# Performance work log

Measured on AMD Instinct MI355X. Metric: run time of the kernel, lower is better.

The kernel has to match this reference:

```python
import jax, jax.numpy as jnp
import numpy as np

LN_EPS = 1e-5

def layer_norm(x, g, b):
    m = x.mean(-1, keepdims=True)
    v = ((x - m) ** 2).mean(-1, keepdims=True)
    return (x - m) / jnp.sqrt(v + LN_EPS) * g + b

def gat_conv(x, src, dst, W, att_src, att_dst, bias, heads, out_ch, concat):
    # PyG GATConv (eval mode, self-loops already included in src/dst).
    N = x.shape[0]
    h = (x @ W).reshape(N, heads, out_ch)                 # [N,H,C]
    a_src = (h * att_src).sum(-1)                          # [N,H]
    a_dst = (h * att_dst).sum(-1)                          # [N,H]
    e = jax.nn.leaky_relu(a_src[src] + a_dst[dst], 0.2)   # [E,H]
    emax = jax.ops.segment_max(e, dst, num_segments=N)    # [N,H]
    ee = jnp.exp(e - emax[dst])
    denom = jax.ops.segment_sum(ee, dst, num_segments=N)  # [N,H]
    alpha = ee / (denom[dst] + 1e-16)                      # [E,H]
    out = jax.ops.segment_sum(alpha[:, :, None] * h[src], dst, num_segments=N)  # [N,H,C]
    out = out.reshape(N, heads * out_ch) if concat else out.mean(axis=1)
    return out + bias

def setup_inputs() -> dict:
    key = jax.random.key(0)
    ks = jax.random.split(key, 32)
    N, G, E = 50000, 405, 300000
    RH, GH, H = 256, 256, 4
    def w(k, shape, fan_in):
        return jax.random.normal(k, shape, dtype=jnp.float32) * (1.0 / np.sqrt(fan_in))
    d = {}
    d["x"] = jax.random.normal(ks[0], (N, G), dtype=jnp.float32)
    d["edge_index"] = jax.random.randint(ks[1], (2, E), 0, N, dtype=jnp.int64)
    # JointEncoder
    d["enc_w1"] = w(ks[2], (G, RH), G); d["enc_b1"] = jnp.zeros(RH)
    d["ln1_g"] = jnp.ones(RH); d["ln1_b"] = jnp.zeros(RH)
    d["enc_w2"] = w(ks[3], (RH, RH), RH); d["enc_b2"] = jnp.zeros(RH)
    d["ln2_g"] = jnp.ones(RH); d["ln2_b"] = jnp.zeros(RH)
    d["w1"] = w(ks[4], (RH, H * GH), RH)
    d["att_src1"] = w(ks[5], (H, GH), GH); d["att_dst1"] = w(ks[6], (H, GH), GH)
    d["bias1"] = jnp.zeros(H * GH)
    d["res1_w"] = w(ks[7], (RH, H * GH), RH); d["res1_b"] = jnp.zeros(H * GH)
    d["w2"] = w(ks[8], (H * GH, 2 * 96), H * GH)
    d["att_src2"] = w(ks[9], (2, 96), 96); d["att_dst2"] = w(ks[10], (2, 96), 96)
    d["bias2"] = jnp.zeros(2 * 96)
    d["res2_w"] = w(ks[11], (H * GH, 2 * 96), H * GH); d["res2_b"] = jnp.zeros(2 * 96)
    d["w3"] = w(ks[12], (192, 128), 192)
    d["att_src3"] = w(ks[13], (1, 128), 128); d["att_dst3"] = w(ks[14], (1, 128), 128)
    d["bias3"] = jnp.zeros(128)
    d["res3_w"] = w(ks[15], (192, 128), 192); d["res3_b"] = jnp.zeros(128)
    # MLP head
    d["mlp_w1"] = w(ks[16], (128, 64), 128); d["mlp_b1"] = jnp.zeros(64)
    d["mlp_w2"] = w(ks[17], (64, 2), 64); d["mlp_b2"] = jnp.zeros(2)
    return d

def reference(x, edge_index, enc_w1, enc_b1, ln1_g, ln1_b, enc_w2, enc_b2, ln2_g, ln2_b,
              w1, att_src1, att_dst1, bias1, res1_w, res1_b,
              w2, att_src2, att_dst2, bias2, res2_w, res2_b,
              w3, att_src3, att_dst3, bias3, res3_w, res3_b,
              mlp_w1, mlp_b1, mlp_w2, mlp_b2):
    N = x.shape[0]
    loop = jnp.arange(N, dtype=edge_index.dtype)
    src = jnp.concatenate([edge_index[0], loop])
    dst = jnp.concatenate([edge_index[1], loop])
    # JointEncoder (eval: dropout is identity)
    h = jax.nn.relu(layer_norm(x @ enc_w1 + enc_b1, ln1_g, ln1_b))
    h = jax.nn.relu(layer_norm(h @ enc_w2 + enc_b2, ln2_g, ln2_b))
    # Block 1
    idn = h
    h = jax.nn.elu(gat_conv(h, src, dst, w1, att_src1, att_dst1, bias1, 4, 256, True))
    h = h + (idn @ res1_w + res1_b)
    # Block 2
    idn = h
    h = jax.nn.elu(gat_conv(h, src, dst, w2, att_src2, att_dst2, bias2, 2, 96, True))
    h = h + (idn @ res2_w + res2_b)
    # Block 3
    idn = h
    h = jax.nn.elu(gat_conv(h, src, dst, w3, att_src3, att_dst3, bias3, 1, 128, False))
    h = h + (idn @ res3_w + res3_b)
    # MLP head
    out = jax.nn.relu(h @ mlp_w1 + mlp_b1) @ mlp_w2 + mlp_b2
    return out
```

## Files before the change

kernel.cpp:

```cpp
#include <hip/hip_runtime.h>
#include <cstddef>

#define LN_EPS 1e-5f

typedef __bf16 bf16x8 __attribute__((ext_vector_type(8)));
typedef float  f32x4  __attribute__((ext_vector_type(4)));

typedef __attribute__((address_space(3))) unsigned int lds_u32;
typedef __attribute__((address_space(1))) unsigned int glb_u32;

__device__ __forceinline__ void gl2lds16(const void* g, void* l) {
    __builtin_amdgcn_global_load_lds((const glb_u32*)g, (lds_u32*)l, 16, 0, 0);
}

__device__ __forceinline__ float b2f(ushort h) {
    return __uint_as_float(((unsigned)h) << 16);
}
__device__ __forceinline__ ushort f2b(float f) {
    unsigned u = __float_as_uint(f);
    return (ushort)((u + 0x7fffu + ((u >> 16) & 1u)) >> 16);
}
__device__ __forceinline__ unsigned pack2(float lo, float hi) {
    return (unsigned)f2b(lo) | ((unsigned)f2b(hi) << 16);
}
__device__ __forceinline__ uint2 pack4(const f32x4 v) {
    return make_uint2(pack2(v[0], v[1]), pack2(v[2], v[3]));
}

__device__ __forceinline__ void xcd_map(int& bx, int& by) {
    int NX = gridDim.x, MBr = gridDim.y;
    int L = blockIdx.y * NX + blockIdx.x;
    int G = NX * 8;
    int g = L / G;
    if (g * 8 + 8 <= MBr) {
        int r = L - g * G;
        by = g * 8 + (r & 7);
        bx = r >> 3;
    } else {
        by = L / NX;
        bx = L - by * NX;
    }
}

__device__ __forceinline__ float wave_allreduce_max(float v) {
    #pragma unroll
    for (int off = 32; off > 0; off >>= 1) v = fmaxf(v, __shfl_xor(v, off, 64));
    return v;
}
__device__ __forceinline__ float wave_allreduce_sum(float v) {
    #pragma unroll
    for (int off = 32; off > 0; off >>= 1) v += __shfl_xor(v, off, 64);
    return v;
}

__device__ __forceinline__ void stage3(const ushort* a0, const ushort* a1, const ushort* b0,
                                       ushort* __restrict__ As, ushort* __restrict__ Bs,
                                       int lb) {
    gl2lds16(a0, As + lb);
    gl2lds16(a1, As + lb + 4096);
    gl2lds16(b0, Bs + lb);
}

__device__ __forceinline__ void mfma_loop256(const ushort* aA0, const ushort* aA1,
                                             const ushort* aB0,
                                             ushort* __restrict__ As, ushort* __restrict__ Bs,
                                             int lb,
                                             int K, int wr, int wc, int cA, int l15,
                                             f32x4 acc[4][4]) {
    const int BUFA = 256 * 32;
    const int BUFB = 128 * 32;
    const int nk = K >> 5;
    stage3(aA0, aA1, aB0, As, Bs, lb);
    int p = 0;
    for (int t = 0; t < nk; t++) {
        asm volatile("s_waitcnt vmcnt(0)" ::: "memory");
        __builtin_amdgcn_s_barrier();
        __builtin_amdgcn_sched_barrier(0);
        int kn = (t + 1) * 32;
        if (kn < K) stage3(aA0 + kn, aA1 + kn, aB0 + kn,
                           As + (p ^ 1) * BUFA, Bs + (p ^ 1) * BUFB, lb);
        const ushort* Ac = As + p * BUFA;
        const ushort* Bc = Bs + p * BUFB;
        bf16x8 af[4], bf[4];
        #pragma unroll
        for (int i = 0; i < 4; i++)
            af[i] = *reinterpret_cast<const bf16x8*>(&Ac[(wr + i * 16 + l15) * 32 + cA]);
        #pragma unroll
        for (int j = 0; j < 4; j++)
            bf[j] = *reinterpret_cast<const bf16x8*>(&Bc[(wc + j * 16 + l15) * 32 + cA]);
        #pragma unroll
        for (int i = 0; i < 4; i++)
            #pragma unroll
            for (int j = 0; j < 4; j++)
                acc[i][j] = __builtin_amdgcn_mfma_f32_16x16x32_bf16(bf[j], af[i], acc[i][j], 0, 0, 0);
        p ^= 1;
    }
    __syncthreads();
}

template<int EPI>
__global__ __launch_bounds__(512, 4) void bgemm(const ushort* __restrict__ A,
                                                const ushort* __restrict__ BT,
                                                const float* __restrict__ bias,
                                                void* __restrict__ out, int ldc,
                                                float* __restrict__ Rf,
                                                float* __restrict__ Sf, int Fs,
                                                int M, int Ncols, int K, int lda) {
    __shared__ ushort As[2][256 * 32];
    __shared__ ushort Bs[2][128 * 32];
    const int tid = threadIdx.x;
    int bx, by; xcd_map(bx, by);
    const int m0 = by * 256, n0 = bx * 128;
    const int w = tid >> 6, lane = tid & 63;
    const int wr = (w >> 1) * 64, wc = (w & 1) * 64;
    const int quad = lane >> 4, l15 = lane & 15;
    const int cA = (quad ^ ((l15 >> 1) & 3)) * 8;
    const int lb = w * 512;

    const int r = tid >> 2, g = ((tid & 3) ^ ((tid >> 3) & 3)) * 8;
    int ga0 = m0 + r;       if (ga0 >= M) ga0 = M - 1;
    int ga1 = m0 + 128 + r; if (ga1 >= M) ga1 = M - 1;
    const ushort* aA0 = A + (size_t)ga0 * lda + g;
    const ushort* aA1 = A + (size_t)ga1 * lda + g;
    const ushort* aB0 = BT + (size_t)(n0 + r) * K + g;

    f32x4 acc[4][4] = {};
    mfma_loop256(aA0, aA1, aB0, As[0], Bs[0], lb, K, wr, wc, cA, l15, acc);

    if (EPI == 4) {
        if (wc == 0) {
            #pragma unroll
            for (int i = 0; i < 4; i++) {
                float o0 = 0.f, o1 = 0.f;
                #pragma unroll
                for (int j = 0; j < 4; j++) {
                    int colbase = j * 16 + quad * 4;
                    float4 bv = *reinterpret_cast<const float4*>(&bias[colbase]);
                    float bb[4] = { bv.x, bv.y, bv.z, bv.w };
                    #pragma unroll
                    for (int rr = 0; rr < 4; rr++) {
                        float vv = fmaxf(acc[i][j][rr] + bb[rr], 0.f);
                        int c = colbase + rr;
                        o0 += vv * Rf[2 * c];
                        o1 += vv * Rf[2 * c + 1];
                    }
                }
                o0 += __shfl_xor(o0, 16, 64); o0 += __shfl_xor(o0, 32, 64);
                o1 += __shfl_xor(o1, 16, 64); o1 += __shfl_xor(o1, 32, 64);
                int row = m0 + wr + i * 16 + l15;
                if (quad == 0 && row < M) {
                    ((float*)out)[(size_t)row * 2]     = o0 + Sf[0];
                    ((float*)out)[(size_t)row * 2 + 1] = o1 + Sf[1];
                }
            }
        }
        return;
    }

    const int twoH = Ncols - 2 * Fs;
    #pragma unroll
    for (int i = 0; i < 4; i++) {
        int row = m0 + wr + i * 16 + l15;
        if (row >= M) continue;
        #pragma unroll
        for (int j = 0; j < 4; j++) {
            int colbase = n0 + wc + j * 16 + quad * 4;
            if (EPI == 0) {
                f32x4 v = acc[i][j];
                if (bias) {
                    float4 bv = *reinterpret_cast<const float4*>(&bias[colbase]);
                    v[0] += bv.x; v[1] += bv.y; v[2] += bv.z; v[3] += bv.w;
                }
                *reinterpret_cast<f32x4*>(&((float*)out)[(size_t)row * ldc + colbase]) = v;
            } else if (EPI == 5) {
                if (colbase + 3 < Fs) {
                    *reinterpret_cast<uint2*>(&((ushort*)out)[(size_t)row * Fs + colbase]) = pack4(acc[i][j]);
                } else if (colbase >= Fs && colbase + 3 < 2 * Fs) {
                    *reinterpret_cast<f32x4*>(&Rf[(size_t)row * Fs + (colbase - Fs)]) = acc[i][j];
                } else {
                    #pragma unroll
                    for (int rr = 0; rr < 4; rr++) {
                        int col = colbase + rr;
                        if (col < 2 * Fs || col >= Ncols) continue;
                        Sf[(size_t)row * twoH + (col - 2 * Fs)] = acc[i][j][rr];
                    }
                }
            }
        }
    }
}

__global__ __launch_bounds__(512, 4) void bgemm_b1(const ushort* __restrict__ accb,
                                                   const ushort* __restrict__ w1T,
                                                   const ushort* __restrict__ h1b,
                                                   const ushort* __restrict__ res1T,
                                                   const float* __restrict__ bias1,
                                                   const float* __restrict__ res1b,
                                                   ushort* __restrict__ H2b, int M) {
    __shared__ ushort As[2][256 * 32];
    __shared__ ushort Bs[2][128 * 32];
    const int tid = threadIdx.x;
    int bx, by; xcd_map(bx, by);
    const int m0 = by * 256, n0 = bx * 128;
    const int h = n0 >> 8;
    const int w = tid >> 6, lane = tid & 63;
    const int wr = (w >> 1) * 64, wc = (w & 1) * 64;
    const int quad = lane >> 4, l15 = lane & 15;
    const int cA = (quad ^ ((l15 >> 1) & 3)) * 8;
    const int lb = w * 512;

    const int r = tid >> 2, g = ((tid & 3) ^ ((tid >> 3) & 3)) * 8;
    int ga0 = m0 + r;       if (ga0 >= M) ga0 = M - 1;
    int ga1 = m0 + 128 + r; if (ga1 >= M) ga1 = M - 1;

    f32x4 acc[4][4] = {};

    mfma_loop256(accb + (size_t)ga0 * 1024 + h * 256 + g,
                 accb + (size_t)ga1 * 1024 + h * 256 + g,
                 w1T + (size_t)(n0 + r) * 256 + g,
                 As[0], Bs[0], lb, 256, wr, wc, cA, l15, acc);

    #pragma unroll
    for (int i = 0; i < 4; i++) {
        #pragma unroll
        for (int j = 0; j < 4; j++) {
            int colbase = n0 + wc + j * 16 + quad * 4;
            float4 bv = *reinterpret_cast<const float4*>(&bias1[colbase]);
            float4 rv = *reinterpret_cast<const float4*>(&res1b[colbase]);
            float bb[4] = { bv.x, bv.y, bv.z, bv.w };
            float rr[4] = { rv.x, rv.y, rv.z, rv.w };
            #pragma unroll
            for (int q = 0; q < 4; q++) {
                float t = acc[i][j][q] + bb[q];
                t = t > 0.f ? t : (__expf(t) - 1.f);
                acc[i][j][q] = t + rr[q];
            }
        }
    }

    mfma_loop256(h1b + (size_t)ga0 * 256 + g,
                 h1b + (size_t)ga1 * 256 + g,
                 res1T + (size_t)(n0 + r) * 256 + g,
                 As[0], Bs[0], lb, 256, wr, wc, cA, l15, acc);

    #pragma unroll
    for (int i = 0; i < 4; i++) {
        int row = m0 + wr + i * 16 + l15;
        if (row >= M) continue;
        #pragma unroll
        for (int j = 0; j < 4; j++) {
            int colbase = n0 + wc + j * 16 + quad * 4;
            *reinterpret_cast<uint2*>(&H2b[(size_t)row * 1024 + colbase]) = pack4(acc[i][j]);
        }
    }
}

__global__ void conv_pad_x_kernel(const float* __restrict__ x, ushort* __restrict__ xb, int N) {
    int t = blockIdx.x * 256 + threadIdx.x;
    if (t >= N * 448) return;
    int n = t / 448, k = t - n * 448;
    xb[t] = f2b(k < 405 ? x[(size_t)n * 405 + k] : 0.f);
}

#define PREP_PB 5135
__device__ __forceinline__ void prep_seg(int t, const float* src, ushort* dst,
                                         int K, int Nreal, int Kpad, int ldsrc) {
    int n = t / Kpad, k = t - n * Kpad;
    float v = (k < K && n < Nreal) ? src[(size_t)k * ldsrc + n] : 0.f;
    dst[t] = f2b(v);
}

__global__ void prep_fold_kernel(const float* __restrict__ enc_w1, const float* __restrict__ enc_w2,
                                 const float* __restrict__ w1, const float* __restrict__ res1_w,
                                 const float* __restrict__ w2, const float* __restrict__ res2_w,
                                 const float* __restrict__ w3, const float* __restrict__ res3_w,
                                 const float* __restrict__ mlp_w1,
                                 const float* __restrict__ att_s1, const float* __restrict__ att_d1,
                                 const float* __restrict__ att_s2, const float* __restrict__ att_d2,
                                 const float* __restrict__ att_s3, const float* __restrict__ att_d3,
                                 ushort* __restrict__ enc_w1T, ushort* __restrict__ enc_w2T,
                                 ushort* __restrict__ w1T, ushort* __restrict__ res1T,
                                 ushort* __restrict__ Bcat2T, ushort* __restrict__ Bcat3T,
                                 ushort* __restrict__ mlpw1T,
                                 float* __restrict__ qs, float* __restrict__ qd) {
    int blk = blockIdx.x;
    if (blk < PREP_PB) {
        int t = blk * 256 + threadIdx.x;
        const int c0 = 114688;
        const int c1 = c0 + 65536;
        const int c2 = c1 + 262144;
        const int c3 = c2 + 262144;
        const int c4 = c3 + 196608;
        const int c5 = c4 + 196608;
        const int c6 = c5 + 126976;
        const int c7 = c6 + 24576;
        const int c8 = c7 + 24576;
        const int c9 = c8 + 24192;
        const int c10 = c9 + 16384;
        if (t < c0)      prep_seg(t,        enc_w1, enc_w1T, 405, 256, 448, 256);
        else if (t < c1) prep_seg(t - c0,   enc_w2, enc_w2T, 256, 256, 256, 256);
        else if (t < c2) prep_seg(t - c1,   w1,     w1T,     256, 1024, 256, 1024);
        else if (t < c3) prep_seg(t - c2,   res1_w, res1T,   256, 1024, 256, 1024);
        else if (t < c4) prep_seg(t - c3,   w2,     Bcat2T,  1024, 192, 1024, 192);
        else if (t < c5) prep_seg(t - c4,   res2_w, Bcat2T + (size_t)192 * 1024, 1024, 192, 1024, 192);
        else if (t < c6) Bcat2T[(size_t)388 * 1024 + (t - c5)] = 0;
        else if (t < c7) prep_seg(t - c6,   w3,     Bcat3T,  192, 128, 192, 128);
        else if (t < c8) prep_seg(t - c7,   res3_w, Bcat3T + (size_t)128 * 192, 192, 128, 192, 128);
        else if (t < c9) Bcat3T[(size_t)258 * 192 + (t - c8)] = 0;
        else if (t < c10) prep_seg(t - c9,  mlp_w1, mlpw1T,  128, 64, 128, 64);
        return;
    }
    int fw = (blk - PREP_PB) * 4 + (threadIdx.x >> 6);
    int lane = threadIdx.x & 63;
    if (fw < 1024) {
        int h = fw >> 8, k = fw & 255;
        const float* wrow = w1 + (size_t)k * 1024 + h * 256;
        f32x4 wv = *reinterpret_cast<const f32x4*>(&wrow[lane * 4]);
        f32x4 as = *reinterpret_cast<const f32x4*>(&att_s1[h * 256 + lane * 4]);
        f32x4 ad = *reinterpret_cast<const f32x4*>(&att_d1[h * 256 + lane * 4]);
        float ss = wv[0] * as[0] + wv[1] * as[1] + wv[2] * as[2] + wv[3] * as[3];
        float sd = wv[0] * ad[0] + wv[1] * ad[1] + wv[2] * ad[2] + wv[3] * ad[3];
        ss = wave_allreduce_sum(ss);
        sd = wave_allreduce_sum(sd);
        if (lane == 0) { qs[fw] = ss; qd[fw] = sd; }
    } else if (fw < 1024 + 2048) {
        int t = fw - 1024;
        int h = t >> 10, k = t & 1023;
        const float* wrow = w2 + (size_t)k * 192 + h * 96;
        const float* as = att_s2 + h * 96;
        const float* ad = att_d2 + h * 96;
        float w0 = wrow[lane];
        float ss = w0 * as[lane], sd = w0 * ad[lane];
        if (lane < 32) {
            float w1v = wrow[64 + lane];
            ss += w1v * as[64 + lane];
            sd += w1v * ad[64 + lane];
        }
        ss = wave_allreduce_sum(ss);
        sd = wave_allreduce_sum(sd);
        if (lane == 0) {
            Bcat2T[(size_t)384 * 1024 + t] = f2b(ss);
            Bcat2T[(size_t)386 * 1024 + t] = f2b(sd);
        }
    } else {
        int t = fw - 3072;
        if (t < 192) {
            const float* wrow = w3 + (size_t)t * 128;
            float w0 = wrow[lane], w1v = wrow[64 + lane];
            float ss = w0 * att_s3[lane] + w1v * att_s3[64 + lane];
            float sd = w0 * att_d3[lane] + w1v * att_d3[64 + lane];
            ss = wave_allreduce_sum(ss);
            sd = wave_allreduce_sum(sd);
            if (lane == 0) {
                Bcat3T[(size_t)256 * 192 + t] = f2b(ss);
                Bcat3T[(size_t)257 * 192 + t] = f2b(sd);
            }
        }
    }
}

template<int H>
__global__ __launch_bounds__(256) void ln_relu_w_kernel(const float* __restrict__ x,
                                                        const float* __restrict__ g,
                                                        const float* __restrict__ b,
                                                        const float* __restrict__ qs,
                                                        const float* __restrict__ qd,
                                                        ushort* __restrict__ out,
                                                        float* __restrict__ a_s,
                                                        float* __restrict__ a_d,
                                                        int N) {
    const int lane = threadIdx.x & 63;
    int wid = blockIdx.x * 4 + (threadIdx.x >> 6);
    const int nw = gridDim.x * 4;
    const int c4 = lane * 4;

    f32x4 gv = *reinterpret_cast<const f32x4*>(&g[c4]);
    f32x4 bv = *reinterpret_cast<const f32x4*>(&b[c4]);
    f32x4 qsv[H > 0 ? H : 1], qdv[H > 0 ? H : 1];
    if (H > 0) {
        #pragma unroll
        for (int hh = 0; hh < H; hh++) {
            qsv[hh] = *reinterpret_cast<const f32x4*>(&qs[hh * 256 + c4]);
            qdv[hh] = *reinterpret_cast<const f32x4*>(&qd[hh * 256 + c4]);
        }
    }

    for (int r0 = wid * 2; r0 < N; r0 += 2 * nw) {
        int r1 = r0 + 1;
        bool has1 = r1 < N;
        f32x4 va = *reinterpret_cast<const f32x4*>(&x[(size_t)r0 * 256 + c4]);
        f32x4 vb = has1 ? *reinterpret_cast<const f32x4*>(&x[(size_t)r1 * 256 + c4]) : va;
        float sa  = va[0] + va[1] + va[2] + va[3];
        float s2a = va[0] * va[0] + va[1] * va[1] + va[2] * va[2] + va[3] * va[3];
        float sb  = vb[0] + vb[1] + vb[2] + vb[3];
        float s2b = vb[0] * vb[0] + vb[1] * vb[1] + vb[2] * vb[2] + vb[3] * vb[3];
        #pragma unroll
        for (int off = 32; off > 0; off >>= 1) {
            sa  += __shfl_xor(sa,  off, 64);
            sb  += __shfl_xor(sb,  off, 64);
            s2a += __shfl_xor(s2a, off, 64);
            s2b += __shfl_xor(s2b, off, 64);
        }
        float ma  = sa * (1.f / 256.f);
        float mb  = sb * (1.f / 256.f);
        float rsa = rsqrtf(s2a * (1.f / 256.f) - ma * ma + LN_EPS);
        float rsb = rsqrtf(s2b * (1.f / 256.f) - mb * mb + LN_EPS);
        f32x4 oa, ob;
        #pragma unroll
        for (int k = 0; k < 4; k++) {
            oa[k] = fmaxf((va[k] - ma) * rsa * gv[k] + bv[k], 0.f);
            ob[k] = fmaxf((vb[k] - mb) * rsb * gv[k] + bv[k], 0.f);
        }
        *reinterpret_cast<uint2*>(&out[(size_t)r0 * 256 + c4]) =
            make_uint2(pack2(oa[0], oa[1]), pack2(oa[2], oa[3]));
        if (has1)
            *reinterpret_cast<uint2*>(&out[(size_t)r1 * 256 + c4]) =
                make_uint2(pack2(ob[0], ob[1]), pack2(ob[2], ob[3]));
        if (H > 0) {
            float sc[H > 0 ? 4 * H : 1];
            #pragma unroll
            for (int hh = 0; hh < H; hh++) {
                sc[hh]           = oa[0] * qsv[hh][0] + oa[1] * qsv[hh][1] + oa[2] * qsv[hh][2] + oa[3] * qsv[hh][3];
                sc[H + hh]       = oa[0] * qdv[hh][0] + oa[1] * qdv[hh][1] + oa[2] * qdv[hh][2] + oa[3] * qdv[hh][3];
                sc[2 * H + hh]   = ob[0] * qsv[hh][0] + ob[1] * qsv[hh][1] + ob[2] * qsv[hh][2] + ob[3] * qsv[hh][3];
                sc[3 * H + hh]   = ob[0] * qdv[hh][0] + ob[1] * qdv[hh][1] + ob[2] * qdv[hh][2] + ob[3] * qdv[hh][3];
            }
            #pragma unroll
            for (int off = 32; off > 0; off >>= 1)
                #pragma unroll
                for (int k = 0; k < 4 * H; k++) sc[k] += __shfl_xor(sc[k], off, 64);
            if (lane == 0) {
                #pragma unroll
                for (int k = 0; k < H; k++) a_s[(size_t)r0 * H + k] = sc[k];
                if (has1)
                    #pragma unroll
                    for (int k = 0; k < H; k++) a_s[(size_t)r1 * H + k] = sc[2 * H + k];
            } else if (lane == 1) {
                #pragma unroll
                for (int k = 0; k < H; k++) a_d[(size_t)r0 * H + k] = sc[H + k];
                if (has1)
                    #pragma unroll
                    for (int k = 0; k < H; k++) a_d[(size_t)r1 * H + k] = sc[3 * H + k];
            }
        }
    }
}

__device__ __forceinline__ void edge_sd(const int* ei, int e, int E, int& s, int& d) {
    if (e < E) { s = ei[e]; d = ei[E + e]; } else { s = d = e - E; }
}

__global__ void deg_kernel(const int* __restrict__ ei, int* __restrict__ deg, int E, int Et) {
    int e = blockIdx.x * blockDim.x + threadIdx.x;
    if (e >= Et) return;
    int s, d; edge_sd(ei, e, E, s, d);
    atomicAdd(&deg[d], 1);
}

__global__ __launch_bounds__(256) void scan1_kernel(const int* __restrict__ deg,
                                                    int* __restrict__ incl,
                                                    int* __restrict__ part, int N) {
    __shared__ int sd[256];
    int t = threadIdx.x;
    int i = blockIdx.x * 256 + t;
    int v = (i < N) ? deg[i] : 0;
    sd[t] = v; __syncthreads();
    #pragma unroll
    for (int o = 1; o < 256; o <<= 1) {
        int x = (t >= o) ? sd[t - o] : 0;
        __syncthreads();
        sd[t] += x;
        __syncthreads();
    }
    if (i < N) incl[i] = sd[t];
    if (t == 255) part[blockIdx.x] = sd[255];
}

__global__ __launch_bounds__(256) void scan2_kernel(int* __restrict__ part, int nb) {
    __shared__ int sd[256];
    int t = threadIdx.x;
    int v = (t < nb) ? part[t] : 0;
    sd[t] = v; __syncthreads();
    #pragma unroll
    for (int o = 1; o < 256; o <<= 1) {
        int x = (t >= o) ? sd[t - o] : 0;
        __syncthreads();
        sd[t] += x;
        __syncthreads();
    }
    if (t < nb) part[t] = sd[t];
}

__global__ void scan3_kernel(const int* __restrict__ incl, const int* __restrict__ deg,
                             const int* __restrict__ part, int* __restrict__ row_ptr, int N) {
    int i = blockIdx.x * blockDim.x + threadIdx.x;
    if (i >= N) return;
    int off = (blockIdx.x > 0) ? part[blockIdx.x - 1] : 0;
    row_ptr[i] = incl[i] - deg[i] + off;
}

__global__ void fill_kernel(const int* __restrict__ ei, const int* __restrict__ row_ptr,
                            int* __restrict__ cur, int* __restrict__ csr_src, int E, int Et) {
    int e = blockIdx.x * blockDim.x + threadIdx.x;
    if (e >= Et) return;
    int s, d; edge_sd(ei, e, E, s, d);
    int pos = row_ptr[d] + atomicAdd(&cur[d], 1);
    csr_src[pos] = s;
}

#define ACAP 256

__global__ __launch_bounds__(128) void aggr_b1_fused_kernel(const int* __restrict__ row_ptr,
                                                            const int* __restrict__ deg,
                                                            const int* __restrict__ csr_src,
                                                            const float* __restrict__ a_s,
                                                            const float* __restrict__ a_d,
                                                            const ushort* __restrict__ h1b,
                                                            ushort* __restrict__ accb) {
    __shared__ float alf[ACAP][4];
    __shared__ float sstat[8];
    int d = blockIdx.x, t = threadIdx.x;
    int base = row_ptr[d], dg = deg[d];
    float4 ad = *reinterpret_cast<const float4*>(&a_d[(size_t)d * 4]);
    {
        const int hb = (t >> 6) * 2;
        const int l = t & 63;
        const float ad0 = hb ? ad.z : ad.x;
        const float ad1 = hb ? ad.w : ad.y;
        float m0 = -1e30f, m1 = -1e30f;
        for (int j = l; j < dg; j += 64) {
            int s = csr_src[base + j];
            float2 sv = *reinterpret_cast<const float2*>(&a_s[(size_t)s * 4 + hb]);
            float c0 = sv.x + ad0; c0 = c0 > 0.f ? c0 : 0.2f * c0; m0 = fmaxf(m0, c0);
            float c1 = sv.y + ad1; c1 = c1 > 0.f ? c1 : 0.2f * c1; m1 = fmaxf(m1, c1);
        }
        m0 = wave_allreduce_max(m0); m1 = wave_allreduce_max(m1);
        float s0 = 0.f, s1 = 0.f;
        for (int j = l; j < dg; j += 64) {
            int s = csr_src[base + j];
            float2 sv = *reinterpret_cast<const float2*>(&a_s[(size_t)s * 4 + hb]);
            float c0 = sv.x + ad0; c0 = c0 > 0.f ? c0 : 0.2f * c0; float e0 = __expf(c0 - m0); s0 += e0;
            float c1 = sv.y + ad1; c1 = c1 > 0.f ? c1 : 0.2f * c1; float e1 = __expf(c1 - m1); s1 += e1;
            if (j < ACAP) { alf[j][hb] = e0; alf[j][hb + 1] = e1; }
        }
        s0 = wave_allreduce_sum(s0); s1 = wave_allreduce_sum(s1);
        if (l == 0) {
            sstat[hb] = m0; sstat[hb + 1] = m1;
            sstat[4 + hb] = 1.f / (s0 + 1e-16f); sstat[5 + hb] = 1.f / (s1 + 1e-16f);
        }
    }
    __syncthreads();
    float r0 = sstat[4], r1 = sstat[5], r2 = sstat[6], r3 = sstat[7];
    float a00 = 0, a01 = 0, a10 = 0, a11 = 0, a20 = 0, a21 = 0, a30 = 0, a31 = 0;

    auto alpha4 = [&](int j, int s, float& al0, float& al1, float& al2, float& al3) {
        if (j < ACAP) {
            al0 = alf[j][0] * r0; al1 = alf[j][1] * r1;
            al2 = alf[j][2] * r2; al3 = alf[j][3] * r3;
        } else {
            float4 sv = *reinterpret_cast<const float4*>(&a_s[(size_t)s * 4]);
            float c0 = sv.x + ad.x; c0 = c0 > 0.f ? c0 : 0.2f * c0; al0 = __expf(c0 - sstat[0]) * r0;
            float c1 = sv.y + ad.y; c1 = c1 > 0.f ? c1 : 0.2f * c1; al1 = __expf(c1 - sstat[1]) * r1;
            float c2 = sv.z + ad.z; c2 = c2 > 0.f ? c2 : 0.2f * c2; al2 = __expf(c2 - sstat[2]) * r2;
            float c3 = sv.w + ad.w; c3 = c3 > 0.f ? c3 : 0.2f * c3; al3 = __expf(c3 - sstat[3]) * r3;
        }
    };
    int j = 0;
    for (; j + 2 <= dg; j += 2) {
        int s0i = csr_src[base + j], s1i = csr_src[base + j + 1];
        unsigned v0 = reinterpret_cast<const unsigned*>(h1b + (size_t)s0i * 256)[t];
        unsigned v1 = reinterpret_cast<const unsigned*>(h1b + (size_t)s1i * 256)[t];
        float x0, x1, x2, x3, y0, y1, y2, y3;
        alpha4(j, s0i, x0, x1, x2, x3);
        alpha4(j + 1, s1i, y0, y1, y2, y3);
        float lo0 = b2f((ushort)(v0 & 0xffff)), hi0 = b2f((ushort)(v0 >> 16));
        float lo1 = b2f((ushort)(v1 & 0xffff)), hi1 = b2f((ushort)(v1 >> 16));
        a00 += x0 * lo0 + y0 * lo1; a01 += x0 * hi0 + y0 * hi1;
        a10 += x1 * lo0 + y1 * lo1; a11 += x1 * hi0 + y1 * hi1;
        a20 += x2 * lo0 + y2 * lo1; a21 += x2 * hi0 + y2 * hi1;
        a30 += x3 * lo0 + y3 * lo1; a31 += x3 * hi0 + y3 * hi1;
    }
    if (j < dg) {
        int s0i = csr_src[base + j];
        unsigned v0 = reinterpret_cast<const unsigned*>(h1b + (size_t)s0i * 256)[t];
        float x0, x1, x2, x3;
        alpha4(j, s0i, x0, x1, x2, x3);
        float lo0 = b2f((ushort)(v0 & 0xffff)), hi0 = b2f((ushort)(v0 >> 16));
        a00 += x0 * lo0; a01 += x0 * hi0;
        a10 += x1 * lo0; a11 += x1 * hi0;
        a20 += x2 * lo0; a21 += x2 * hi0;
        a30 += x3 * lo0; a31 += x3 * hi0;
    }
    unsigned* o = reinterpret_cast<unsigned*>(accb + (size_t)d * 1024);
    o[t]       = pack2(a00, a01);
    o[t + 128] = pack2(a10, a11);
    o[t + 256] = pack2(a20, a21);
    o[t + 384] = pack2(a30, a31);
}

template<int H, int C, int F, int NT>
__global__ __launch_bounds__(NT) void aggr_comb_fused_kernel(const int* __restrict__ row_ptr,
                                                             const int* __restrict__ deg,
                                                             const int* __restrict__ csr_src,
                                                             const float* __restrict__ as,
                                                             const ushort* __restrict__ g,
                                                             const float* __restrict__ Rf,
                                                             const float* __restrict__ gb,
                                                             const float* __restrict__ rb,
                                                             ushort* __restrict__ outb) {
    __shared__ float alf[ACAP][H];
    __shared__ float sstat[2 * H];
    int d = blockIdx.x;
    int t = threadIdx.x;
    int base = row_ptr[d], dg = deg[d];
    if (t < 64) {
        float ad[H], mx[H];
        #pragma unroll
        for (int h = 0; h < H; h++) { ad[h] = as[(size_t)d * 2 * H + H + h]; mx[h] = -1e30f; }
        for (int j = t; j < dg; j += 64) {
            int s = csr_src[base + j];
            #pragma unroll
            for (int h = 0; h < H; h++) {
                float c = as[(size_t)s * 2 * H + h] + ad[h];
                c = c > 0.f ? c : 0.2f * c;
                mx[h] = fmaxf(mx[h], c);
            }
        }
        #pragma unroll
        for (int h = 0; h < H; h++) mx[h] = wave_allreduce_max(mx[h]);
        float sm[H];
        #pragma unroll
        for (int h = 0; h < H; h++) sm[h] = 0.f;
        for (int j = t; j < dg; j += 64) {
            int s = csr_src[base + j];
            #pragma unroll
            for (int h = 0; h < H; h++) {
                float c = as[(size_t)s * 2 * H + h] + ad[h];
                c = c > 0.f ? c : 0.2f * c;
                float e = __expf(c - mx[h]);
                sm[h] += e;
                if (j < ACAP) alf[j][h] = e;
            }
        }
        #pragma unroll
        for (int h = 0; h < H; h++) sm[h] = wave_allreduce_sum(sm[h]);
        if (t == 0) {
            #pragma unroll
            for (int h = 0; h < H; h++) { sstat[h] = mx[h]; sstat[H + h] = 1.f / (sm[h] + 1e-16f); }
        }
    }
    __syncthreads();
    int hd = (2 * t) / C;
    float mxv = sstat[hd], rdv = sstat[H + hd];
    float adv = as[(size_t)d * 2 * H + H + hd];
    float lo = 0.f, hi = 0.f;
    auto alpha1 = [&](int j, int s) -> float {
        if (j < ACAP) return alf[j][hd] * rdv;
        float c = as[(size_t)s * 2 * H + hd] + adv;
        c = c > 0.f ? c : 0.2f * c;
        return __expf(c - mxv) * rdv;
    };
    int j = 0;
    for (; j + 2 <= dg; j += 2) {
        int s0 = csr_src[base + j], s1 = csr_src[base + j + 1];
        unsigned v0 = reinterpret_cast<const unsigned*>(g + (size_t)s0 * F)[t];
        unsigned v1 = reinterpret_cast<const unsigned*>(g + (size_t)s1 * F)[t];
        float al0 = alpha1(j, s0), al1 = alpha1(j + 1, s1);
        lo += al0 * b2f((ushort)(v0 & 0xffff)) + al1 * b2f((ushort)(v1 & 0xffff));
        hi += al0 * b2f((ushort)(v0 >> 16))    + al1 * b2f((ushort)(v1 >> 16));
    }
    if (j < dg) {
        int s0 = csr_src[base + j];
        unsigned v0 = reinterpret_cast<const unsigned*>(g + (size_t)s0 * F)[t];
        float al0 = alpha1(j, s0);
        lo += al0 * b2f((ushort)(v0 & 0xffff));
        hi += al0 * b2f((ushort)(v0 >> 16));
    }
    int c0 = 2 * t, c1 = 2 * t + 1;
    float o0 = lo + gb[c0]; o0 = o0 > 0.f ? o0 : (__expf(o0) - 1.f);
    float o1 = hi + gb[c1]; o1 = o1 > 0.f ? o1 : (__expf(o1) - 1.f);
    o0 += Rf[(size_t)d * F + c0] + rb[c0];
    o1 += Rf[(size_t)d * F + c1] + rb[c1];
    reinterpret_cast<unsigned*>(outb)[(size_t)d * (F / 2) + t] = pack2(o0, o1);
}

extern "C" void kernel_launch(void* const* d_in, const int* in_sizes, int n_in,
                              void* d_out, int out_size, void* d_ws, size_t ws_size,
                              hipStream_t stream) {
    const float* x        = (const float*)d_in[0];
    const int*   ei       = (const int*)d_in[1];
    const float* enc_w1   = (const float*)d_in[2];
    const float* enc_b1   = (const float*)d_in[3];
    const float* ln1_g    = (const float*)d_in[4];
    const float* ln1_b    = (const float*)d_in[5];
    const float* enc_w2   = (const float*)d_in[6];
    const float* enc_b2   = (const float*)d_in[7];
    const float* ln2_g    = (const float*)d_in[8];
    const float* ln2_b    = (const float*)d_in[9];
    const float* w1       = (const float*)d_in[10];
    const float* att_src1 = (const float*)d_in[11];
    const float* att_dst1 = (const float*)d_in[12];
    const float* bias1    = (const float*)d_in[13];
    const float* res1_w   = (const float*)d_in[14];
    const float* res1_b   = (const float*)d_in[15];
    const float* w2       = (const float*)d_in[16];
    const float* att_src2 = (const float*)d_in[17];
    const float* att_dst2 = (const float*)d_in[18];
    const float* bias2    = (const float*)d_in[19];
    const float* res2_w   = (const float*)d_in[20];
    const float* res2_b   = (const float*)d_in[21];
    const float* w3       = (const float*)d_in[22];
    const float* att_src3 = (const float*)d_in[23];
    const float* att_dst3 = (const float*)d_in[24];
    const float* bias3    = (const float*)d_in[25];
    const float* res3_w   = (const float*)d_in[26];
    const float* res3_b   = (const float*)d_in[27];
    const float* mlp_w1   = (const float*)d_in[28];
    const float* mlp_b1   = (const float*)d_in[29];
    const float* mlp_w2   = (const float*)d_in[30];
    const float* mlp_b2   = (const float*)d_in[31];

    const int N  = in_sizes[0] / 405;
    const int E  = in_sizes[1] / 2;
    const int Et = E + N;
    const int NB = (N + 255) / 256;

    char* p = (char*)d_ws;
    char* R0 = p;
    char* R1 = R0 + (size_t)N * 896;
    char* R2 = R1 + (size_t)N * 512;
    char* R3 = R2 + (size_t)N * 512;
    char* R4 = R3 + (size_t)N * 2048;
    char* T  = R4 + (size_t)N * 2048;

    ushort* xb   = (ushort*)R0;
    ushort* H3b  = (ushort*)R0;
    ushort* h0b  = (ushort*)R1;
    ushort* G2b  = (ushort*)R1;
    ushort* h1b  = (ushort*)R2;
    ushort* G3b  = (ushort*)R2;
    ushort* H4b  = (ushort*)(R2 + (size_t)N * 256);
    float*  F1   = (float*)R3;
    ushort* H2b  = (ushort*)R3;
    ushort* accb = (ushort*)R4;
    float*  Rf   = (float*)R4;

    float* a_s   = (float*)T;                         T += (size_t)N * 4 * 4;
    float* a_d   = (float*)T;                         T += (size_t)N * 4 * 4;
    float* qs    = (float*)T;                         T += 2048 * 4;
    float* qd    = (float*)T;                         T += 2048 * 4;
    int* deg     = (int*)T;                           T += (size_t)N * 4;
    int* cur     = (int*)T;                           T += (size_t)N * 4;
    int* row_ptr = (int*)T;                           T += (size_t)N * 4;
    int* incl    = (int*)T;                           T += (size_t)N * 4;
    int* part    = (int*)T;                           T += 256 * 4;
    int* csr_src = (int*)T;                           T += (size_t)Et * 4;
    ushort* enc_w1T = (ushort*)T;                     T += (size_t)256 * 448 * 2;
    ushort* enc_w2T = (ushort*)T;                     T += (size_t)256 * 256 * 2;
    ushort* w1T     = (ushort*)T;                     T += (size_t)1024 * 256 * 2;
    ushort* res1T   = (ushort*)T;                     T += (size_t)1024 * 256 * 2;
    ushort* Bcat2T  = (ushort*)T;                     T += (size_t)512 * 1024 * 2;
    ushort* Bcat3T  = (ushort*)T;                     T += (size_t)384 * 192 * 2;
    ushort* mlpw1T  = (ushort*)T;                     T += (size_t)128 * 128 * 2;

    auto cdiv = [](int a, int b) { return (a + b - 1) / b; };
    const int MBr = cdiv(N, 256);

    (void)hipMemsetAsync(deg, 0, (size_t)N * 8, stream);
    deg_kernel<<<cdiv(Et, 256), 256, 0, stream>>>(ei, deg, E, Et);
    scan1_kernel<<<NB, 256, 0, stream>>>(deg, incl, part, N);
    scan2_kernel<<<1, 256, 0, stream>>>(part, NB);
    scan3_kernel<<<NB, 256, 0, stream>>>(incl, deg, part, row_ptr, N);
    fill_kernel<<<cdiv(Et, 256), 256, 0, stream>>>(ei, row_ptr, cur, csr_src, E, Et);

    prep_fold_kernel<<<PREP_PB + 816, 256, 0, stream>>>(
        enc_w1, enc_w2, w1, res1_w, w2, res2_w, w3, res3_w, mlp_w1,
        att_src1, att_dst1, att_src2, att_dst2, att_src3, att_dst3,
        enc_w1T, enc_w2T, w1T, res1T, Bcat2T, Bcat3T, mlpw1T, qs, qd);

    conv_pad_x_kernel<<<cdiv(N * 448, 256), 256, 0, stream>>>(x, xb, N);
    bgemm<0><<<dim3(2, MBr), 512, 0, stream>>>(xb, enc_w1T, enc_b1, F1, 256, nullptr, nullptr, 0, N, 256, 448, 448);
    ln_relu_w_kernel<0><<<2048, 256, 0, stream>>>(F1, ln1_g, ln1_b, nullptr, nullptr, h0b, nullptr, nullptr, N);
    bgemm<0><<<dim3(2, MBr), 512, 0, stream>>>(h0b, enc_w2T, enc_b2, F1, 256, nullptr, nullptr, 0, N, 256, 256, 256);
    ln_relu_w_kernel<4><<<2048, 256, 0, stream>>>(F1, ln2_g, ln2_b, qs, qd, h1b, a_s, a_d, N);

    aggr_b1_fused_kernel<<<N, 128, 0, stream>>>(row_ptr, deg, csr_src, a_s, a_d, h1b, accb);
    bgemm_b1<<<dim3(8, MBr), 512, 0, stream>>>(accb, w1T, h1b, res1T, bias1, res1_b, H2b, N);

    {
        bgemm<5><<<dim3(4, MBr), 512, 0, stream>>>(H2b, Bcat2T, nullptr, G2b, 0, Rf, a_s, 192, N, 388, 1024, 1024);
        aggr_comb_fused_kernel<2, 96, 192, 96><<<N, 96, 0, stream>>>(row_ptr, deg, csr_src, a_s,
                                                                     G2b, Rf, bias2, res2_b, H3b);
    }

    {
        bgemm<5><<<dim3(3, MBr), 512, 0, stream>>>(H3b, Bcat3T, nullptr, G3b, 0, Rf, a_s, 128, N, 258, 192, 192);
        aggr_comb_fused_kernel<1, 128, 128, 64><<<N, 64, 0, stream>>>(row_ptr, deg, csr_src, a_s,
                                                                      G3b, Rf, bias3, res3_b, H4b);
    }

    bgemm<4><<<dim3(1, MBr), 512, 0, stream>>>(H4b, mlpw1T, mlp_b1, d_out, 2,
                                               (float*)mlp_w2, (float*)mlp_b2, 0, N, 64, 128, 128);
}
```

Before: 719.5 us.

## Fold block-2 attention logits into block-1 GEMM epilogue via atomics

Computes the layer-2 attention source/destination scores as fp32 dot products in the bgemm_b1 epilogue, reduced across lanes and accumulated with atomicAdd into a new per-node buffer. The layer-2 GEMM no longer carries the four extra attention columns, so its grid drops from 4 to 3 column blocks. The scores are also taken from fp32 accumulators instead of bf16 outputs. In exchange it adds a memset, extra fp32 loads of the folded vectors, and 8-way contended atomics per row in the epilogue.

Measured after the change: 770.1 us. 1.07x slower.

```diff
diff --git a/kernel.cpp b/kernel.cpp
--- a/kernel.cpp
+++ b/kernel.cpp
@@ -196,6 +196,9 @@
                                                    const ushort* __restrict__ res1T,
                                                    const float* __restrict__ bias1,
                                                    const float* __restrict__ res1b,
+                                                   const float* __restrict__ qs2,
+                                                   const float* __restrict__ qd2,
+                                                   float* __restrict__ as2,
                                                    ushort* __restrict__ H2b, int M) {
     __shared__ ushort As[2][256 * 32];
     __shared__ ushort Bs[2][128 * 32];
@@ -246,11 +249,31 @@
     #pragma unroll
     for (int i = 0; i < 4; i++) {
         int row = m0 + wr + i * 16 + l15;
-        if (row >= M) continue;
+        float p0 = 0.f, p1 = 0.f, p2 = 0.f, p3 = 0.f;
         #pragma unroll
         for (int j = 0; j < 4; j++) {
             int colbase = n0 + wc + j * 16 + quad * 4;
-            *reinterpret_cast<uint2*>(&H2b[(size_t)row * 1024 + colbase]) = pack4(acc[i][j]);
+            float4 v0 = *reinterpret_cast<const float4*>(&qs2[colbase]);
+            float4 v1 = *reinterpret_cast<const float4*>(&qs2[1024 + colbase]);
+            float4 v2 = *reinterpret_cast<const float4*>(&qd2[colbase]);
+            float4 v3 = *reinterpret_cast<const float4*>(&qd2[1024 + colbase]);
+            float a0 = acc[i][j][0], a1 = acc[i][j][1], a2 = acc[i][j][2], a3 = acc[i][j][3];
+            p0 += a0 * v0.x + a1 * v0.y + a2 * v0.z + a3 * v0.w;
+            p1 += a0 * v1.x + a1 * v1.y + a2 * v1.z + a3 * v1.w;
+            p2 += a0 * v2.x + a1 * v2.y + a2 * v2.z + a3 * v2.w;
+            p3 += a0 * v3.x + a1 * v3.y + a2 * v3.z + a3 * v3.w;
+            if (row < M)
+                *reinterpret_cast<uint2*>(&H2b[(size_t)row * 1024 + colbase]) = pack4(acc[i][j]);
+        }
+        p0 += __shfl_xor(p0, 16, 64); p0 += __shfl_xor(p0, 32, 64);
+        p1 += __shfl_xor(p1, 16, 64); p1 += __shfl_xor(p1, 32, 64);
+        p2 += __shfl_xor(p2, 16, 64); p2 += __shfl_xor(p2, 32, 64);
+        p3 += __shfl_xor(p3, 16, 64); p3 += __shfl_xor(p3, 32, 64);
+        if (quad == 0 && row < M) {
+            atomicAdd(&as2[(size_t)row * 4 + 0], p0);
+            atomicAdd(&as2[(size_t)row * 4 + 1], p1);
+            atomicAdd(&as2[(size_t)row * 4 + 2], p2);
+            atomicAdd(&as2[(size_t)row * 4 + 3], p3);
         }
     }
 }
@@ -282,7 +305,8 @@
                                  ushort* __restrict__ w1T, ushort* __restrict__ res1T,
                                  ushort* __restrict__ Bcat2T, ushort* __restrict__ Bcat3T,
                                  ushort* __restrict__ mlpw1T,
-                                 float* __restrict__ qs, float* __restrict__ qd) {
+                                 float* __restrict__ qs, float* __restrict__ qd,
+                                 float* __restrict__ qs2, float* __restrict__ qd2) {
     int blk = blockIdx.x;
     if (blk < PREP_PB) {
         int t = blk * 256 + threadIdx.x;
@@ -339,8 +363,8 @@
         ss = wave_allreduce_sum(ss);
         sd = wave_allreduce_sum(sd);
         if (lane == 0) {
-            Bcat2T[(size_t)384 * 1024 + t] = f2b(ss);
-            Bcat2T[(size_t)386 * 1024 + t] = f2b(sd);
+            qs2[t] = ss;
+            qd2[t] = sd;
         }
     } else {
         int t = fw - 3072;
@@ -749,6 +773,9 @@
     float* a_d   = (float*)T;                         T += (size_t)N * 4 * 4;
     float* qs    = (float*)T;                         T += 2048 * 4;
     float* qd    = (float*)T;                         T += 2048 * 4;
+    float* qs2   = (float*)T;                         T += 2048 * 4;
+    float* qd2   = (float*)T;                         T += 2048 * 4;
+    float* as2   = (float*)T;                         T += (size_t)N * 4 * 4;
     int* deg     = (int*)T;                           T += (size_t)N * 4;
     int* cur     = (int*)T;                           T += (size_t)N * 4;
     int* row_ptr = (int*)T;                           T += (size_t)N * 4;
@@ -767,6 +794,7 @@
     const int MBr = cdiv(N, 256);
 
     (void)hipMemsetAsync(deg, 0, (size_t)N * 8, stream);
+    (void)hipMemsetAsync(as2, 0, (size_t)N * 16, stream);
     deg_kernel<<<cdiv(Et, 256), 256, 0, stream>>>(ei, deg, E, Et);
     scan1_kernel<<<NB, 256, 0, stream>>>(deg, incl, part, N);
     scan2_kernel<<<1, 256, 0, stream>>>(part, NB);
@@ -776,7 +804,7 @@
     prep_fold_kernel<<<PREP_PB + 816, 256, 0, stream>>>(
         enc_w1, enc_w2, w1, res1_w, w2, res2_w, w3, res3_w, mlp_w1,
         att_src1, att_dst1, att_src2, att_dst2, att_src3, att_dst3,
-        enc_w1T, enc_w2T, w1T, res1T, Bcat2T, Bcat3T, mlpw1T, qs, qd);
+        enc_w1T, enc_w2T, w1T, res1T, Bcat2T, Bcat3T, mlpw1T, qs, qd, qs2, qd2);
 
     conv_pad_x_kernel<<<cdiv(N * 448, 256), 256, 0, stream>>>(x, xb, N);
     bgemm<0><<<dim3(2, MBr), 512, 0, stream>>>(xb, enc_w1T, enc_b1, F1, 256, nullptr, nullptr, 0, N, 256, 448, 448);
@@ -785,11 +813,12 @@
     ln_relu_w_kernel<4><<<2048, 256, 0, stream>>>(F1, ln2_g, ln2_b, qs, qd, h1b, a_s, a_d, N);
 
     aggr_b1_fused_kernel<<<N, 128, 0, stream>>>(row_ptr, deg, csr_src, a_s, a_d, h1b, accb);
-    bgemm_b1<<<dim3(8, MBr), 512, 0, stream>>>(accb, w1T, h1b, res1T, bias1, res1_b, H2b, N);
+    bgemm_b1<<<dim3(8, MBr), 512, 0, stream>>>(accb, w1T, h1b, res1T, bias1, res1_b,
+                                               qs2, qd2, as2, H2b, N);
 
     {
-        bgemm<5><<<dim3(4, MBr), 512, 0, stream>>>(H2b, Bcat2T, nullptr, G2b, 0, Rf, a_s, 192, N, 388, 1024, 1024);
-        aggr_comb_fused_kernel<2, 96, 192, 96><<<N, 96, 0, stream>>>(row_ptr, deg, csr_src, a_s,
+        bgemm<5><<<dim3(3, MBr), 512, 0, stream>>>(H2b, Bcat2T, nullptr, G2b, 0, Rf, nullptr, 192, N, 384, 1024, 1024);
+        aggr_comb_fused_kernel<2, 96, 192, 96><<<N, 96, 0, stream>>>(row_ptr, deg, csr_src, as2,
                                                                      G2b, Rf, bias2, res2_b, H3b);
     }
 
```
